# Kernel optimization log

Measured on AMD Instinct MI355X. Metric: run time of the kernel, lower is better.

## Reference

```python
import jax, jax.numpy as jnp
import numpy as np

B, C, IMG, P = 8, 6, 384, 16
DIM, HEADS, DEPTH, MLP, NCLS = 768, 12, 4, 3072, 1000
N = (IMG // P) ** 2            # 576 patches
DH = DIM // HEADS              # 64
PATCH_DIM = C * P * P          # 1536


def setup_inputs() -> dict:
    key = jax.random.key(0)
    ks = jax.random.split(key, 13)
    f = lambda k, shp, s=0.02: jax.random.normal(k, shp, jnp.float32) * s
    return {
        "x": jax.random.normal(ks[0], (B, C, IMG, IMG), jnp.float32),
        "patch_w": f(ks[1], (PATCH_DIM, DIM)),
        "patch_b": f(ks[2], (DIM,)),
        "ln1_g": jnp.ones((DEPTH, DIM), jnp.float32),
        "ln1_b": jnp.zeros((DEPTH, DIM), jnp.float32),
        "w_qkv": f(ks[3], (DEPTH, DIM, 3 * DIM)),
        "bias_att": f(ks[4], (DEPTH, HEADS, N, N), 0.5),
        "w_out": f(ks[5], (DEPTH, DIM, DIM)),
        "ln2_g": jnp.ones((DEPTH, DIM), jnp.float32),
        "ln2_b": jnp.zeros((DEPTH, DIM), jnp.float32),
        "w1": f(ks[6], (DEPTH, DIM, MLP)),
        "b1": f(ks[7], (DEPTH, MLP)),
        "w2": f(ks[8], (DEPTH, MLP, DIM)),
        "b2": f(ks[9], (DEPTH, DIM)),
        "lnh_g": jnp.ones((DIM,), jnp.float32),
        "lnh_b": jnp.zeros((DIM,), jnp.float32),
        "w_head": f(ks[10], (DIM, NCLS)),
        "b_head": f(ks[11], (NCLS,)),
    }


def _ln(x, g, b, eps=1e-5):
    m = x.mean(-1, keepdims=True)
    v = ((x - m) ** 2).mean(-1, keepdims=True)
    return (x - m) * jax.lax.rsqrt(v + eps) * g + b


def _patchify(x, patch_w, patch_b):
    # Rearrange 'b c (h p1) (w p2) -> b (h w) (p1 p2 c)' then Linear(patch_dim, dim)
    b = x.shape[0]
    g = IMG // P
    x = x.reshape(b, C, g, P, g, P).transpose(0, 2, 4, 3, 5, 1).reshape(b, g * g, PATCH_DIM)
    return x @ patch_w + patch_b


def _forward(x, patch_w, patch_b, ln1_g, ln1_b, w_qkv, bias_att, w_out,
             ln2_g, ln2_b, w1, b1, w2, b2, lnh_g, lnh_b, w_head, b_head):
    scale = DH ** -0.5
    tok = _patchify(x, patch_w, patch_b)  # [B, N, DIM]; pos_info='mul_att_normed' -> no pos_embed added

    def block(t, p):
        l1g, l1b, wqkv, bias, wout, l2g, l2b, ww1, bb1, ww2, bb2 = p
        h = _ln(t, l1g, l1b)
        qkv = h @ wqkv                                     # [B, N, 3*DIM]
        q, k, v = jnp.split(qkv, 3, axis=-1)
        rs = lambda a: a.reshape(t.shape[0], N, HEADS, DH).transpose(0, 2, 1, 3)
        q, k, v = rs(q), rs(k), rs(v)                      # [B, H, N, DH]
        dots = jnp.einsum('bhid,bhjd->bhij', q, k) * scale
        # mul_att_normed: softmax(qk) * softmax(bias), renormalized over keys
        attn = jax.nn.softmax(dots, axis=-1) * jax.nn.softmax(bias, axis=-1)[None]
        attn = attn / attn.sum(-1, keepdims=True)
        o = jnp.einsum('bhij,bhjd->bhid', attn, v)
        o = o.transpose(0, 2, 1, 3).reshape(t.shape[0], N, DIM) @ wout
        t = t + o
        h2 = _ln(t, l2g, l2b)
        t = t + (jax.nn.gelu(h2 @ ww1 + bb1, approximate=False) @ ww2 + bb2)
        return t, None

    tok, _ = jax.lax.scan(block, tok,
                          (ln1_g, ln1_b, w_qkv, bias_att, w_out,
                           ln2_g, ln2_b, w1, b1, w2, b2))
    pooled = tok.mean(axis=1)                              # mean-pool tokens
    return _ln(pooled, lnh_g, lnh_b) @ w_head + b_head     # [B, NCLS]


def reference(x, patch_w, patch_b, ln1_g, ln1_b, w_qkv, bias_att, w_out,
              ln2_g, ln2_b, w1, b1, w2, b2, lnh_g, lnh_b, w_head, b_head):
    return _forward(x, patch_w, patch_b, ln1_g, ln1_b, w_qkv, bias_att, w_out,
                    ln2_g, ln2_b, w1, b1, w2, b2, lnh_g, lnh_b, w_head, b_head)
```

## Files before the change

kernel.cpp:

```cpp
#include <hip/hip_runtime.h>
#include <hip/hip_bf16.h>

typedef __attribute__((ext_vector_type(8))) short bf16x8;
typedef __attribute__((ext_vector_type(4))) float f32x4;

#define DEVI __device__ __forceinline__

DEVI unsigned short f2bf_bits(float f) {
    __hip_bfloat16 h = __float2bfloat16(f);
    return *reinterpret_cast<unsigned short*>(&h);
}
DEVI float bfbits2f(unsigned short u) {
    __hip_bfloat16 h = *reinterpret_cast<__hip_bfloat16*>(&u);
    return __bfloat162float(h);
}

DEVI void gload_lds16(const void* g, void* lds) {
    __builtin_amdgcn_global_load_lds(
        (const __attribute__((address_space(1))) unsigned int*)g,
        (__attribute__((address_space(3))) unsigned int*)lds, 16, 0, 0);
}

template <int N> DEVI void wait_vm() {
    if constexpr (N == 0) asm volatile("s_waitcnt vmcnt(0)" ::: "memory");
    else if constexpr (N == 4) asm volatile("s_waitcnt vmcnt(4)" ::: "memory");
    else if constexpr (N == 6) asm volatile("s_waitcnt vmcnt(6)" ::: "memory");
    else if constexpr (N == 12) asm volatile("s_waitcnt vmcnt(12)" ::: "memory");
    __builtin_amdgcn_sched_barrier(0);
}
DEVI void lgkm0() {
    asm volatile("s_waitcnt lgkmcnt(0)" ::: "memory");
    __builtin_amdgcn_sched_barrier(0);
}

DEVI int2 remap2d(int bid, int total, int gx) {
    int q = total >> 3, r = total & 7, x = bid & 7, l = bid >> 3;
    int seq = (x < r ? x * (q + 1) : r * (q + 1) + (x - r) * q) + l;
    int g4 = seq / (4 * gx);
    int rem = seq - g4 * 4 * gx;
    return {g4 * 4 + (rem & 3), rem >> 2};
}
DEVI int2 remap2d_g2(int bid, int total, int gx) {
    int q = total >> 3, r = total & 7, x = bid & 7, l = bid >> 3;
    int seq = (x < r ? x * (q + 1) : r * (q + 1) + (x - r) * q) + l;
    int g2 = seq / (2 * gx);
    int rem = seq - g2 * 2 * gx;
    return {g2 * 2 + (rem & 1), rem >> 1};
}

__global__ __launch_bounds__(256) void patchify_kernel(const float* __restrict__ x,
                                                       unsigned short* __restrict__ patches)
{
    size_t t8 = (size_t)blockIdx.x * 256 + threadIdx.x;
    int jq = (int)(t8 % 48);
    size_t t = t8 / 48;
    int r = (int)(t % 384); t /= 384;
    int c = (int)(t % 6);
    int b = (int)(t / 6);
    int j = jq * 8;
    int gh = r >> 4, p1 = r & 15, gw = j >> 4, p2 = j & 15;
    int prow = b * 576 + gh * 24 + gw;
    int pcol = c * 256 + p1 * 16 + p2;
    const float* src = x + ((((size_t)b * 6 + c) * 384 + r) * 384 + j);
    float4 v0 = ((const float4*)src)[0];
    float4 v1 = ((const float4*)src)[1];
    ushort u[8] = { f2bf_bits(v0.x), f2bf_bits(v0.y), f2bf_bits(v0.z), f2bf_bits(v0.w),
                    f2bf_bits(v1.x), f2bf_bits(v1.y), f2bf_bits(v1.z), f2bf_bits(v1.w) };
    *(int4*)&patches[(size_t)prow * 1536 + pcol] = *(int4*)u;
}

__global__ __launch_bounds__(256) void convT_patch_kernel(const float* __restrict__ W,
                                                          __hip_bfloat16* __restrict__ Wt)
{
    __shared__ float tile[32][33];
    int n0 = blockIdx.x * 32, kp0 = blockIdx.y * 32;
    int tx = threadIdx.x & 31, ty = threadIdx.x >> 5;
#pragma unroll
    for (int i = 0; i < 4; i++) {
        int kp = kp0 + ty + 8 * i;
        int k = (kp & 255) * 6 + (kp >> 8);
        tile[ty + 8 * i][tx] = W[(size_t)k * 768 + n0 + tx];
    }
    __syncthreads();
#pragma unroll
    for (int i = 0; i < 4; i++)
        Wt[(size_t)(n0 + ty + 8 * i) * 1536 + kp0 + tx] = __float2bfloat16(tile[tx][ty + 8 * i]);
}

DEVI void convT4_dispatch(int bt, const float* wqkv, const float* wout,
                          const float* w1, const float* w2,
                          const float* g1, const float* b1ln,
                          const float* g2, const float* b2ln,
                          __hip_bfloat16* dst, float* part, int tid)
{
    const float* W; const float* gv = nullptr; const float* bv = nullptr;
    __hip_bfloat16* Wt; int K, N, lt, nseg = 0;
    if (bt < 1728)      { W = wqkv; K = 768;  N = 2304; lt = bt;        Wt = dst;           gv = g1; bv = b1ln; nseg = 0; }
    else if (bt < 2304) { W = wout; K = 768;  N = 768;  lt = bt - 1728; Wt = dst + 1769472; }
    else if (bt < 4608) { W = w1;   K = 768;  N = 3072; lt = bt - 2304; Wt = dst + 2359296; gv = g2; bv = b2ln; nseg = 2304; }
    else                { W = w2;   K = 3072; N = 768;  lt = bt - 4608; Wt = dst + 4718592; }
    int tn = N >> 5;
    int k0 = (lt / tn) * 32, n0 = (lt % tn) * 32;

    __shared__ float tile[32][33];
    int tx = tid & 31, ty = tid >> 5;
#pragma unroll
    for (int i = 0; i < 4; i++)
        tile[ty + 8 * i][tx] = W[(size_t)(k0 + ty + 8 * i) * N + n0 + tx];
    __syncthreads();
    float gk = gv ? gv[k0 + tx] : 1.0f;
#pragma unroll
    for (int i = 0; i < 4; i++)
        Wt[(size_t)(n0 + ty + 8 * i) * K + k0 + tx] = __float2bfloat16(tile[tx][ty + 8 * i] * gk);
    if (gv && tid < 64) {
        int nn = tid & 31, j = tid >> 5;
        const float* vec = j ? gv : bv;
        float s = 0.f;
#pragma unroll
        for (int kk = 0; kk < 32; kk++) s += vec[k0 + kk] * tile[kk][nn];
        int kt = k0 >> 5;
        part[((size_t)kt * 2 + j) * 5376 + nseg + n0 + nn] = s;
    }
}

__global__ __launch_bounds__(256) void convT4_kernel(const float* __restrict__ wqkv,
                                                     const float* __restrict__ wout,
                                                     const float* __restrict__ w1,
                                                     const float* __restrict__ w2,
                                                     const float* __restrict__ g1,
                                                     const float* __restrict__ b1ln,
                                                     const float* __restrict__ g2,
                                                     const float* __restrict__ b2ln,
                                                     __hip_bfloat16* __restrict__ dst,
                                                     float* __restrict__ part)
{
    convT4_dispatch(blockIdx.x, wqkv, wout, w1, w2, g1, b1ln, g2, b2ln, dst, part, threadIdx.x);
}

__global__ __launch_bounds__(256) void convT4all_kernel(const float* __restrict__ wqkv,
                                                        const float* __restrict__ wout,
                                                        const float* __restrict__ w1,
                                                        const float* __restrict__ w2,
                                                        const float* __restrict__ ln1_g,
                                                        const float* __restrict__ ln1_b,
                                                        const float* __restrict__ ln2_g,
                                                        const float* __restrict__ ln2_b,
                                                        __hip_bfloat16* __restrict__ dst,
                                                        float* __restrict__ part)
{
    int l = blockIdx.x / 6912, bt = blockIdx.x % 6912;
    convT4_dispatch(bt,
                    wqkv + (size_t)l * 768 * 2304, wout + (size_t)l * 768 * 768,
                    w1 + (size_t)l * 768 * 3072, w2 + (size_t)l * 3072 * 768,
                    ln1_g + l * 768, ln1_b + l * 768, ln2_g + l * 768, ln2_b + l * 768,
                    dst + (size_t)l * 7077888, part + (size_t)l * 258048, threadIdx.x);
}

__global__ __launch_bounds__(256) void lnreduce_kernel(const float* __restrict__ part,
                                                       const float* __restrict__ b1,
                                                       float* __restrict__ coef,
                                                       int lbase)
{
    int l = lbase + blockIdx.y;
    const float* p = part + (size_t)blockIdx.y * 258048;
    int n = blockIdx.x * 256 + threadIdx.x;
    float s1 = 0.f, s2 = 0.f;
    for (int kt = 0; kt < 24; kt++) {
        s1 += p[((size_t)kt * 2 + 0) * 5376 + n];
        s2 += p[((size_t)kt * 2 + 1) * 5376 + n];
    }
    float* dst = coef + (size_t)l * 10752;
    if (n < 2304) { dst[n] = s1; dst[2304 + n] = s2; }
    else {
        int n0 = n - 2304;
        dst[4608 + n0] = s1 + b1[(size_t)l * 3072 + n0];
        dst[4608 + 3072 + n0] = s2;
    }
}

__global__ __launch_bounds__(256) void stats_kernel(const __hip_bfloat16* __restrict__ tok,
                                                    float2* __restrict__ stats)
{
    int row = blockIdx.x * 4 + (threadIdx.x >> 6);
    int lane = threadIdx.x & 63;
    const unsigned short* tr = (const unsigned short*)(tok + (size_t)row * 768) + lane * 12;
    float s = 0.f, s2 = 0.f;
#pragma unroll
    for (int i = 0; i < 3; i++) {
        ushort4 u = ((const ushort4*)tr)[i];
        float v0 = bfbits2f(u.x), v1 = bfbits2f(u.y), v2 = bfbits2f(u.z), v3 = bfbits2f(u.w);
        s += v0 + v1 + v2 + v3;
        s2 += v0 * v0 + v1 * v1 + v2 * v2 + v3 * v3;
    }
#pragma unroll
    for (int m = 32; m >= 1; m >>= 1) { s += __shfl_xor(s, m); s2 += __shfl_xor(s2, m); }
    if (lane == 0) {
        float mean = s * (1.0f / 768.0f);
        float var = s2 * (1.0f / 768.0f) - mean * mean;
        stats[row] = make_float2(mean, rsqrtf(var + 1e-5f));
    }
}

__global__ __launch_bounds__(192) void lnf_kernel(const float* __restrict__ x,
                                                  const float* __restrict__ g,
                                                  const float* __restrict__ b,
                                                  float* __restrict__ out)
{
    int row = blockIdx.x, tid = threadIdx.x;
    float4 v4 = *(const float4*)&x[(size_t)row * 768 + tid * 4];
    float v[4] = {v4.x, v4.y, v4.z, v4.w};
    float s = v[0] + v[1] + v[2] + v[3];
    float s2 = v[0] * v[0] + v[1] * v[1] + v[2] * v[2] + v[3] * v[3];
#pragma unroll
    for (int m = 32; m >= 1; m >>= 1) { s += __shfl_xor(s, m); s2 += __shfl_xor(s2, m); }
    __shared__ float red[6];
    int w = tid >> 6;
    if ((tid & 63) == 0) { red[w] = s; red[3 + w] = s2; }
    __syncthreads();
    s = red[0] + red[1] + red[2];
    s2 = red[3] + red[4] + red[5];
    float mean = s * (1.0f / 768.0f);
    float var = s2 * (1.0f / 768.0f) - mean * mean;
    float rstd = rsqrtf(var + 1e-5f);
    float4 g4 = *(const float4*)&g[tid * 4];
    float4 b4 = *(const float4*)&b[tid * 4];
    float o[4] = { (v[0] - mean) * rstd * g4.x + b4.x, (v[1] - mean) * rstd * g4.y + b4.y,
                   (v[2] - mean) * rstd * g4.z + b4.z, (v[3] - mean) * rstd * g4.w + b4.w };
    *(float4*)&out[(size_t)row * 768 + tid * 4] = make_float4(o[0], o[1], o[2], o[3]);
}

template <bool GELU>
__global__ __launch_bounds__(512, 2) void gemm_8ph_kernel(
    const __hip_bfloat16* __restrict__ A,
    const __hip_bfloat16* __restrict__ Bt,
    const float2* __restrict__ stats,
    const float* __restrict__ c1v,
    const float* __restrict__ c2v,
    __hip_bfloat16* __restrict__ Cb,
    int M, int N, int K, int gx)
{
    __shared__ __align__(16) __hip_bfloat16 AsF[32768];
    __shared__ __align__(16) __hip_bfloat16 BsF[32768];
    const int tid = threadIdx.x;
    const int wid = tid >> 6, lane = tid & 63;
    const int g = lane >> 4, l16 = lane & 15;
    const int wmh = wid >> 2, wnn = wid & 3;

    int2 bc = remap2d_g2(blockIdx.x, gridDim.x, gx);
    const int bm = bc.x * 256, bn = bc.y * 256;

    const int srow = tid >> 2;
    size_t aS[2], bS[2];
#pragma unroll
    for (int i = 0; i < 2; i++) {
        int row = i * 128 + srow;
        int lc = (tid & 3) ^ ((row >> 1) & 3);
        aS[i] = (size_t)(bm + row) * K + lc * 8;
        bS[i] = (size_t)(bn + row) * K + lc * 8;
    }
    auto stageA = [&](int buf, int kh, int tq) {
        const __hip_bfloat16* ap = A + (size_t)tq * 64 + kh * 32;
        __hip_bfloat16* dst = AsF + (buf * 2 + kh) * 8192;
        gload_lds16(ap + aS[0], dst + tid * 8);
        gload_lds16(ap + aS[1], dst + 4096 + tid * 8);
    };
    auto stageB = [&](int buf, int kh, int tq) {
        const __hip_bfloat16* bp = Bt + (size_t)tq * 64 + kh * 32;
        __hip_bfloat16* dst = BsF + (buf * 2 + kh) * 8192;
        gload_lds16(bp + bS[0], dst + tid * 8);
        gload_lds16(bp + bS[1], dst + 4096 + tid * 8);
    };

    const int csw = (l16 >> 1) & 3;
    const int rdo = (g ^ csw) << 3;
    const int aBase = (wmh * 128 + l16) * 32 + rdo;
    const int bBase = (wnn * 64 + l16) * 32 + rdo;

    f32x4 acc[8][4] = {};
    const int nt = K >> 6;

    stageA(0, 0, 0); stageB(0, 0, 0); stageA(0, 1, 0); stageB(0, 1, 0);
    stageA(1, 0, 1); stageB(1, 0, 1);
    wait_vm<4>();
    __builtin_amdgcn_s_barrier();
    __builtin_amdgcn_sched_barrier(0);

    bf16x8 af[8], bf2[2];
    for (int t = 0; t < nt; t++) {
        const int b = t & 1;
        const int k0 = (b * 2 + 0) * 8192, k1 = (b * 2 + 1) * 8192;

#pragma unroll
        for (int mi = 0; mi < 8; mi++) af[mi] = *(const bf16x8*)&AsF[k0 + aBase + mi * 512];
        bf2[0] = *(const bf16x8*)&BsF[k0 + bBase + 0 * 512];
        bf2[1] = *(const bf16x8*)&BsF[k0 + bBase + 1 * 512];
        if (t + 1 < nt) stageA(b ^ 1, 1, t + 1);
        __builtin_amdgcn_s_barrier(); lgkm0();
        __builtin_amdgcn_s_setprio(1);
#pragma unroll
        for (int mi = 0; mi < 8; mi++) {
            acc[mi][0] = __builtin_amdgcn_mfma_f32_16x16x32_bf16(af[mi], bf2[0], acc[mi][0], 0, 0, 0);
            acc[mi][1] = __builtin_amdgcn_mfma_f32_16x16x32_bf16(af[mi], bf2[1], acc[mi][1], 0, 0, 0);
        }
        __builtin_amdgcn_s_setprio(0);
        __builtin_amdgcn_s_barrier();

        bf2[0] = *(const bf16x8*)&BsF[k0 + bBase + 2 * 512];
        bf2[1] = *(const bf16x8*)&BsF[k0 + bBase + 3 * 512];
        if (t + 1 < nt) stageB(b ^ 1, 1, t + 1);
        __builtin_amdgcn_s_barrier(); lgkm0();
        __builtin_amdgcn_s_setprio(1);
#pragma unroll
        for (int mi = 0; mi < 8; mi++) {
            acc[mi][2] = __builtin_amdgcn_mfma_f32_16x16x32_bf16(af[mi], bf2[0], acc[mi][2], 0, 0, 0);
            acc[mi][3] = __builtin_amdgcn_mfma_f32_16x16x32_bf16(af[mi], bf2[1], acc[mi][3], 0, 0, 0);
        }
        __builtin_amdgcn_s_setprio(0);
        __builtin_amdgcn_s_barrier();

#pragma unroll
        for (int mi = 0; mi < 8; mi++) af[mi] = *(const bf16x8*)&AsF[k1 + aBase + mi * 512];
        bf2[0] = *(const bf16x8*)&BsF[k1 + bBase + 0 * 512];
        bf2[1] = *(const bf16x8*)&BsF[k1 + bBase + 1 * 512];
        if (t + 2 < nt) stageA(b, 0, t + 2);
        __builtin_amdgcn_s_barrier(); lgkm0();
        __builtin_amdgcn_s_setprio(1);
#pragma unroll
        for (int mi = 0; mi < 8; mi++) {
            acc[mi][0] = __builtin_amdgcn_mfma_f32_16x16x32_bf16(af[mi], bf2[0], acc[mi][0], 0, 0, 0);
            acc[mi][1] = __builtin_amdgcn_mfma_f32_16x16x32_bf16(af[mi], bf2[1], acc[mi][1], 0, 0, 0);
        }
        __builtin_amdgcn_s_setprio(0);
        __builtin_amdgcn_s_barrier();

        bf2[0] = *(const bf16x8*)&BsF[k1 + bBase + 2 * 512];
        bf2[1] = *(const bf16x8*)&BsF[k1 + bBase + 3 * 512];
        if (t + 2 < nt) stageB(b, 0, t + 2);
        __builtin_amdgcn_s_barrier(); lgkm0();
        __builtin_amdgcn_s_setprio(1);
#pragma unroll
        for (int mi = 0; mi < 8; mi++) {
            acc[mi][2] = __builtin_amdgcn_mfma_f32_16x16x32_bf16(af[mi], bf2[0], acc[mi][2], 0, 0, 0);
            acc[mi][3] = __builtin_amdgcn_mfma_f32_16x16x32_bf16(af[mi], bf2[1], acc[mi][3], 0, 0, 0);
        }
        __builtin_amdgcn_s_setprio(0);
        if (t + 2 < nt) wait_vm<4>();
        else            wait_vm<0>();
        __builtin_amdgcn_s_barrier();
        __builtin_amdgcn_sched_barrier(0);
    }

    __hip_bfloat16* scr = AsF + wid * (16 * 72);
#pragma unroll
    for (int mi = 0; mi < 8; mi++) {
        float2 st[4];
#pragma unroll
        for (int r = 0; r < 4; r++)
            st[r] = stats[bm + wmh * 128 + mi * 16 + 4 * g + r];
#pragma unroll
        for (int ni = 0; ni < 4; ni++) {
            int gcol = bn + wnn * 64 + ni * 16 + l16;
            float c1 = c1v[gcol], c2 = c2v[gcol];
#pragma unroll
            for (int r = 0; r < 4; r++) {
                float v = st[r].y * (acc[mi][ni][r] - st[r].x * c2) + c1;
                if (GELU) v = 0.5f * v * (1.0f + erff(v * 0.70710678118654752f));
                scr[(4 * g + r) * 72 + ni * 16 + l16] = __float2bfloat16(v);
            }
        }
        lgkm0();
#pragma unroll
        for (int q2 = 0; q2 < 2; q2++) {
            int idx = q2 * 64 + lane;
            int row16 = idx >> 3, ch = idx & 7;
            bf16x8 vv = *(const bf16x8*)&scr[row16 * 72 + ch * 8];
            int grow = bm + wmh * 128 + mi * 16 + row16;
            *(int4*)&Cb[(size_t)grow * N + bn + wnn * 64 + ch * 8] = *(int4*)&vv;
        }
        lgkm0();
    }
}

template <bool BIAS, bool RESID, bool GELU>
__global__ __launch_bounds__(256, 2) void gemm_bt_kernel(
    const __hip_bfloat16* __restrict__ A,
    const __hip_bfloat16* __restrict__ Bt,
    const float* __restrict__ bias,
    const __hip_bfloat16* __restrict__ resid,
    __hip_bfloat16* __restrict__ Cb,
    int M, int N, int K, int gx)
{
    constexpr int BM = 64;
    __shared__ __align__(16) __hip_bfloat16 As[3][BM * 64];
    __shared__ __align__(16) __hip_bfloat16 Bs[3][128 * 64];
    const int tid = threadIdx.x;
    const int wid = tid >> 6, lane = tid & 63;
    const int g = lane >> 4, l16 = lane & 15;
    const int wm = (wid >> 1) * 32, wn = (wid & 1) * 64;

    int2 bc = remap2d(blockIdx.x, gridDim.x, gx);
    const int bm = bc.x * BM, bn = bc.y * 128;

    const int sr32 = tid >> 3, ci = tid & 7;
    const int cg = ci ^ (sr32 & 7);
    const int sdst = tid * 8;
    size_t aOff[2], bOff[4];
#pragma unroll
    for (int i = 0; i < 2; i++) aOff[i] = (size_t)(bm + i * 32 + sr32) * K + cg * 8;
#pragma unroll
    for (int i = 0; i < 4; i++) bOff[i] = (size_t)(bn + i * 32 + sr32) * K + cg * 8;

    auto stage = [&](__hip_bfloat16* asb, __hip_bfloat16* bsb, int tq) {
        const __hip_bfloat16* ap = A + tq * 64;
        const __hip_bfloat16* bp = Bt + tq * 64;
#pragma unroll
        for (int i = 0; i < 2; i++) gload_lds16(ap + aOff[i], asb + i * 2048 + sdst);
#pragma unroll
        for (int i = 0; i < 4; i++) gload_lds16(bp + bOff[i], bsb + i * 2048 + sdst);
    };

    f32x4 acc[2][4] = {};
    const int nt = K >> 6;

    stage(As[0], Bs[0], 0);
    stage(As[1], Bs[1], 1);
    stage(As[2], Bs[2], 2);
    wait_vm<12>();
    __builtin_amdgcn_s_barrier();
    __builtin_amdgcn_sched_barrier(0);

    for (int t = 0; t < nt; t += 3) {
#pragma unroll
        for (int u = 0; u < 3; u++) {
            const int tc = t + u;
            bf16x8 af[2][2], bfr[2][4];
#pragma unroll
            for (int s = 0; s < 2; s++) {
                const int cp = ((s * 4 + g) ^ (l16 & 7)) << 3;
#pragma unroll
                for (int mi = 0; mi < 2; mi++)
                    af[s][mi] = *(const bf16x8*)&As[u][(wm + mi * 16 + l16) * 64 + cp];
#pragma unroll
                for (int ni = 0; ni < 4; ni++)
                    bfr[s][ni] = *(const bf16x8*)&Bs[u][(wn + ni * 16 + l16) * 64 + cp];
            }
#pragma unroll
            for (int s = 0; s < 2; s++)
#pragma unroll
                for (int mi = 0; mi < 2; mi++)
#pragma unroll
                    for (int ni = 0; ni < 4; ni++)
                        acc[mi][ni] = __builtin_amdgcn_mfma_f32_16x16x32_bf16(af[s][mi], bfr[s][ni], acc[mi][ni], 0, 0, 0);

            lgkm0();
            __builtin_amdgcn_s_barrier();
            __builtin_amdgcn_sched_barrier(0);

            if (tc + 3 < nt) stage(As[u], Bs[u], tc + 3);
            if (tc + 1 < nt) {
                if (tc + 4 <= nt)      wait_vm<12>();
                else if (tc + 3 == nt) wait_vm<6>();
                else                   wait_vm<0>();
                __builtin_amdgcn_s_barrier();
                __builtin_amdgcn_sched_barrier(0);
            }
        }
    }

    __hip_bfloat16* scr = &As[0][0] + wid * (16 * 72);
#pragma unroll
    for (int mi = 0; mi < 2; mi++) {
#pragma unroll
        for (int ni = 0; ni < 4; ni++) {
            float bval = 0.0f;
            if (BIAS) bval = bias[bn + wn + ni * 16 + l16];
#pragma unroll
            for (int r = 0; r < 4; r++) {
                float v = acc[mi][ni][r] + bval;
                if (GELU) v = 0.5f * v * (1.0f + erff(v * 0.70710678118654752f));
                scr[(4 * g + r) * 72 + ni * 16 + l16] = __float2bfloat16(v);
            }
        }
        lgkm0();
#pragma unroll
        for (int q2 = 0; q2 < 2; q2++) {
            int row16 = q2 * 8 + (lane >> 3), ch = lane & 7;
            bf16x8 vv = *(const bf16x8*)&scr[row16 * 72 + ch * 8];
            int grow = bm + wm + mi * 16 + row16;
            size_t off = (size_t)grow * N + bn + wn + ch * 8;
            if (RESID) {
                bf16x8 rv = *(const bf16x8*)&resid[off];
#pragma unroll
                for (int e = 0; e < 8; e++)
                    vv[e] = (short)f2bf_bits(bfbits2f((unsigned short)vv[e]) + bfbits2f((unsigned short)rv[e]));
            }
            *(int4*)&Cb[off] = *(int4*)&vv;
        }
        lgkm0();
    }
}

__global__ __launch_bounds__(256) void attn_kernel(const __hip_bfloat16* __restrict__ qkvb,
                                                   const float* __restrict__ bias,
                                                   unsigned short* __restrict__ o)
{
    const int seq = (blockIdx.x & 7) * 108 + (blockIdx.x >> 3);
    const int bb = seq & 7, qt = (seq >> 3) % 9, h = seq / 72;
    const int q0 = qt * 64;
    const int tid = threadIdx.x;
    const int wq = tid >> 6, lane = tid & 63, g = lane >> 4, l16 = lane & 15;

    __shared__ __align__(16) unsigned short Qs[64 * 72];
    __shared__ __align__(16) unsigned short Ks[64 * 72];
    __shared__ __align__(16) unsigned short Vt[64 * 72];
    __shared__ __align__(16) unsigned short Ps[4][16 * 72];

    {
        int r = tid >> 2, cb = (tid & 3) * 16;
        const int4* s4 = (const int4*)&qkvb[(size_t)(bb * 576 + q0 + r) * 2304 + h * 64 + cb];
        int4* d4 = (int4*)&Qs[r * 72 + cb];
        d4[0] = s4[0]; d4[1] = s4[1];
    }
    __syncthreads();
    bf16x8 qf0 = *(const bf16x8*)&Qs[(wq * 16 + l16) * 72 + g * 8];
    bf16x8 qf1 = *(const bf16x8*)&Qs[(wq * 16 + l16) * 72 + 32 + g * 8];

    float m_r[4] = {-1e30f, -1e30f, -1e30f, -1e30f};
    float l_r[4] = {0.f, 0.f, 0.f, 0.f};
    f32x4 oa[4] = {};
    const float* bias_h = bias + (size_t)h * 576 * 576;
    const float scale = 0.125f;

    for (int kt = 0; kt < 576; kt += 64) {
        {
            int r = tid >> 2, cb = (tid & 3) * 16;
            const int4* s4 = (const int4*)&qkvb[(size_t)(bb * 576 + kt + r) * 2304 + 768 + h * 64 + cb];
            int4* d4 = (int4*)&Ks[r * 72 + cb];
            d4[0] = s4[0]; d4[1] = s4[1];
            int key = tid & 63, d0 = (tid >> 6) * 16;
            const unsigned short* vs = (const unsigned short*)&qkvb[(size_t)(bb * 576 + kt + key) * 2304 + 1536 + h * 64 + d0];
            bf16x8 v0 = *(const bf16x8*)vs;
            bf16x8 v1 = *(const bf16x8*)(vs + 8);
#pragma unroll
            for (int e = 0; e < 8; e++) {
                Vt[(d0 + e) * 72 + key] = (unsigned short)v0[e];
                Vt[(d0 + 8 + e) * 72 + key] = (unsigned short)v1[e];
            }
        }
        __syncthreads();

        float bl[4][4];
#pragma unroll
        for (int kc = 0; kc < 4; kc++)
#pragma unroll
            for (int r = 0; r < 4; r++) {
                int q = q0 + wq * 16 + 4 * g + r;
                bl[kc][r] = bias_h[(size_t)q * 576 + kt + kc * 16 + l16];
            }

        f32x4 sc[4] = {};
        __builtin_amdgcn_s_setprio(1);
#pragma unroll
        for (int kc = 0; kc < 4; kc++) {
            bf16x8 kf0 = *(const bf16x8*)&Ks[(kc * 16 + l16) * 72 + g * 8];
            bf16x8 kf1 = *(const bf16x8*)&Ks[(kc * 16 + l16) * 72 + 32 + g * 8];
            sc[kc] = __builtin_amdgcn_mfma_f32_16x16x32_bf16(qf0, kf0, sc[kc], 0, 0, 0);
            sc[kc] = __builtin_amdgcn_mfma_f32_16x16x32_bf16(qf1, kf1, sc[kc], 0, 0, 0);
        }
        __builtin_amdgcn_s_setprio(0);

        float sv[4][4], mt[4] = {-1e30f, -1e30f, -1e30f, -1e30f};
#pragma unroll
        for (int kc = 0; kc < 4; kc++)
#pragma unroll
            for (int r = 0; r < 4; r++) {
                float s = sc[kc][r] * scale + bl[kc][r];
                sv[kc][r] = s;
                mt[r] = fmaxf(mt[r], s);
            }
#pragma unroll
        for (int r = 0; r < 4; r++)
#pragma unroll
            for (int m = 1; m < 16; m <<= 1) mt[r] = fmaxf(mt[r], __shfl_xor(mt[r], m));

        float sf[4];
#pragma unroll
        for (int r = 0; r < 4; r++) {
            float mn = fmaxf(m_r[r], mt[r]);
            sf[r] = __expf(m_r[r] - mn);
            m_r[r] = mn;
        }
        float rs[4] = {0.f, 0.f, 0.f, 0.f};
#pragma unroll
        for (int kc = 0; kc < 4; kc++)
#pragma unroll
            for (int r = 0; r < 4; r++) {
                float p = __expf(sv[kc][r] - m_r[r]);
                rs[r] += p;
                Ps[wq][(4 * g + r) * 72 + kc * 16 + l16] = f2bf_bits(p);
            }
#pragma unroll
        for (int r = 0; r < 4; r++) {
#pragma unroll
            for (int m = 1; m < 16; m <<= 1) rs[r] += __shfl_xor(rs[r], m);
            l_r[r] = l_r[r] * sf[r] + rs[r];
        }
#pragma unroll
        for (int dt = 0; dt < 4; dt++)
#pragma unroll
            for (int r = 0; r < 4; r++) oa[dt][r] *= sf[r];

        asm volatile("s_waitcnt lgkmcnt(0)" ::: "memory");

        __builtin_amdgcn_s_setprio(1);
#pragma unroll
        for (int s = 0; s < 2; s++) {
            bf16x8 pf = *(const bf16x8*)&Ps[wq][l16 * 72 + s * 32 + g * 8];
#pragma unroll
            for (int dt = 0; dt < 4; dt++) {
                bf16x8 vf = *(const bf16x8*)&Vt[(dt * 16 + l16) * 72 + s * 32 + g * 8];
                oa[dt] = __builtin_amdgcn_mfma_f32_16x16x32_bf16(pf, vf, oa[dt], 0, 0, 0);
            }
        }
        __builtin_amdgcn_s_setprio(0);
        __syncthreads();
    }

#pragma unroll
    for (int dt = 0; dt < 4; dt++)
#pragma unroll
        for (int r = 0; r < 4; r++) {
            int q = q0 + wq * 16 + 4 * g + r;
            float v = oa[dt][r] / l_r[r];
            o[(size_t)(bb * 576 + q) * 768 + h * 64 + dt * 16 + l16] = f2bf_bits(v);
        }
}

__global__ __launch_bounds__(256) void pool_kernel(const __hip_bfloat16* __restrict__ tok,
                                                   float* __restrict__ pooled)
{
    int d = blockIdx.x * 256 + threadIdx.x;
    int b = blockIdx.y;
    float s = 0.0f;
    for (int n = 0; n < 576; n++) s += __bfloat162float(tok[(size_t)(b * 576 + n) * 768 + d]);
    pooled[b * 768 + d] = s * (1.0f / 576.0f);
}

__global__ __launch_bounds__(256) void head_kernel(const float* __restrict__ lnp,
                                                   const float* __restrict__ w,
                                                   const float* __restrict__ bh,
                                                   float* __restrict__ out)
{
    int c = blockIdx.x * 256 + threadIdx.x;
    int b = blockIdx.y;
    if (c >= 1000) return;
    float s = bh[c];
    for (int d = 0; d < 768; d++) s += lnp[b * 768 + d] * w[(size_t)d * 1000 + c];
    out[b * 1000 + c] = s;
}

extern "C" void kernel_launch(void* const* d_in, const int* in_sizes, int n_in,
                              void* d_out, int out_size, void* d_ws, size_t ws_size,
                              hipStream_t stream)
{
    const float* x = (const float*)d_in[0];
    const float* patch_w = (const float*)d_in[1];
    const float* patch_b = (const float*)d_in[2];
    const float* ln1_g = (const float*)d_in[3];
    const float* ln1_b = (const float*)d_in[4];
    const float* w_qkv = (const float*)d_in[5];
    const float* bias_att = (const float*)d_in[6];
    const float* w_out = (const float*)d_in[7];
    const float* ln2_g = (const float*)d_in[8];
    const float* ln2_b = (const float*)d_in[9];
    const float* w1 = (const float*)d_in[10];
    const float* b1 = (const float*)d_in[11];
    const float* w2 = (const float*)d_in[12];
    const float* b2 = (const float*)d_in[13];
    const float* lnh_g = (const float*)d_in[14];
    const float* lnh_b = (const float*)d_in[15];
    const float* w_head = (const float*)d_in[16];
    const float* b_head = (const float*)d_in[17];
    float* out = (float*)d_out;

    char* ws = (char*)d_ws;
    __hip_bfloat16* tok = (__hip_bfloat16*)(ws + 0);
    __hip_bfloat16* qkv_bf = (__hip_bfloat16*)(ws + 14155776);
    float* coef = (float*)(ws + 35389440);
    float2* stats = (float2*)(ws + 35561856);
    float* part = (float*)(ws + 35717120);
    float* pooled = (float*)(ws + 56623104);
    float* pooledln = (float*)(ws + 56647680);
    __hip_bfloat16* patches = (__hip_bfloat16*)(ws + 56672256);
    __hip_bfloat16* lw = patches;
    __hip_bfloat16* o_bf = (__hip_bfloat16*)(ws + 77905920);
    __hip_bfloat16* hid_bf = (__hip_bfloat16*)(ws + 84983808);
    __hip_bfloat16* wbuf = (__hip_bfloat16*)(ws + 113295360);
    __hip_bfloat16* lwAll = (__hip_bfloat16*)(ws + 118013952);
    const bool useAll = ws_size >= (size_t)118013952 + 56623104;

    patchify_kernel<<<3456, 256, 0, stream>>>(x, (unsigned short*)patches);
    convT_patch_kernel<<<dim3(24, 48), 256, 0, stream>>>(patch_w, wbuf);
    gemm_bt_kernel<true, false, false><<<432, 256, 0, stream>>>(
        patches, wbuf, patch_b, nullptr, tok, 4608, 768, 1536, 6);

    if (useAll) {
        convT4all_kernel<<<27648, 256, 0, stream>>>(
            w_qkv, w_out, w1, w2, ln1_g, ln1_b, ln2_g, ln2_b, lwAll, part);
        lnreduce_kernel<<<dim3(21, 4), 256, 0, stream>>>(part, b1, coef, 0);
    }

    for (int l = 0; l < 4; l++) {
        __hip_bfloat16* lwl = useAll ? lwAll + (size_t)l * 7077888 : lw;
        const float* cf = coef + (size_t)l * 10752;
        if (!useAll) {
            convT4_kernel<<<6912, 256, 0, stream>>>(
                w_qkv + (size_t)l * 768 * 2304, w_out + (size_t)l * 768 * 768,
                w1 + (size_t)l * 768 * 3072, w2 + (size_t)l * 3072 * 768,
                ln1_g + l * 768, ln1_b + l * 768, ln2_g + l * 768, ln2_b + l * 768, lw, part);
            lnreduce_kernel<<<dim3(21, 1), 256, 0, stream>>>(part, b1, coef, l);
        }
        stats_kernel<<<1152, 256, 0, stream>>>(tok, stats);
        gemm_8ph_kernel<false><<<162, 512, 0, stream>>>(
            tok, lwl, stats, cf, cf + 2304, qkv_bf, 4608, 2304, 768, 9);
        attn_kernel<<<864, 256, 0, stream>>>(
            qkv_bf, bias_att + (size_t)l * 12 * 576 * 576, (unsigned short*)o_bf);
        gemm_bt_kernel<false, true, false><<<432, 256, 0, stream>>>(
            o_bf, lwl + 1769472, nullptr, tok, tok, 4608, 768, 768, 6);
        stats_kernel<<<1152, 256, 0, stream>>>(tok, stats);
        gemm_8ph_kernel<true><<<216, 512, 0, stream>>>(
            tok, lwl + 2359296, stats, cf + 4608, cf + 4608 + 3072, hid_bf, 4608, 3072, 768, 12);
        gemm_bt_kernel<true, true, false><<<432, 256, 0, stream>>>(
            hid_bf, lwl + 4718592, b2 + l * 768, tok, tok, 4608, 768, 3072, 6);
    }

    pool_kernel<<<dim3(3, 8), 256, 0, stream>>>(tok, pooled);
    lnf_kernel<<<8, 192, 0, stream>>>(pooled, lnh_g, lnh_b, pooledln);
    head_kernel<<<dim3(4, 8), 256, 0, stream>>>(pooledln, w_head, b_head, out);
}
```

Before: 840.8 us.

## Fuse LayerNorm row statistics into GEMM A-fragment loop, drop stats kernel

Removes the standalone stats_kernel launches before the QKV and MLP-up GEMMs. Wave column 0 of each workgroup accumulates row sum and sum-of-squares from the A fragments it already loads, reduces them across lane groups, and stores per-row mean/rstd in LDS for the epilogue. This saves two launches and one read of the token tensor per layer. In exchange it adds VALU work on one wave per phase, which can stall the other waves at the barriers, plus an extra syncthreads before the epilogue.

```diff
diff --git a/kernel.cpp b/kernel.cpp
--- a/kernel.cpp
+++ b/kernel.cpp
@@ -178,29 +178,6 @@
     }
 }
 
-__global__ __launch_bounds__(256) void stats_kernel(const __hip_bfloat16* __restrict__ tok,
-                                                    float2* __restrict__ stats)
-{
-    int row = blockIdx.x * 4 + (threadIdx.x >> 6);
-    int lane = threadIdx.x & 63;
-    const unsigned short* tr = (const unsigned short*)(tok + (size_t)row * 768) + lane * 12;
-    float s = 0.f, s2 = 0.f;
-#pragma unroll
-    for (int i = 0; i < 3; i++) {
-        ushort4 u = ((const ushort4*)tr)[i];
-        float v0 = bfbits2f(u.x), v1 = bfbits2f(u.y), v2 = bfbits2f(u.z), v3 = bfbits2f(u.w);
-        s += v0 + v1 + v2 + v3;
-        s2 += v0 * v0 + v1 * v1 + v2 * v2 + v3 * v3;
-    }
-#pragma unroll
-    for (int m = 32; m >= 1; m >>= 1) { s += __shfl_xor(s, m); s2 += __shfl_xor(s2, m); }
-    if (lane == 0) {
-        float mean = s * (1.0f / 768.0f);
-        float var = s2 * (1.0f / 768.0f) - mean * mean;
-        stats[row] = make_float2(mean, rsqrtf(var + 1e-5f));
-    }
-}
-
 __global__ __launch_bounds__(192) void lnf_kernel(const float* __restrict__ x,
                                                   const float* __restrict__ g,
                                                   const float* __restrict__ b,
@@ -233,7 +210,6 @@
 __global__ __launch_bounds__(512, 2) void gemm_8ph_kernel(
     const __hip_bfloat16* __restrict__ A,
     const __hip_bfloat16* __restrict__ Bt,
-    const float2* __restrict__ stats,
     const float* __restrict__ c1v,
     const float* __restrict__ c2v,
     __hip_bfloat16* __restrict__ Cb,
@@ -277,6 +253,7 @@
     const int bBase = (wnn * 64 + l16) * 32 + rdo;
 
     f32x4 acc[8][4] = {};
+    float s1a[8] = {}, s2a[8] = {};
     const int nt = K >> 6;
 
     stageA(0, 0, 0); stageB(0, 0, 0); stageA(0, 1, 0); stageB(0, 1, 0);
@@ -303,6 +280,18 @@
             acc[mi][1] = __builtin_amdgcn_mfma_f32_16x16x32_bf16(af[mi], bf2[1], acc[mi][1], 0, 0, 0);
         }
         __builtin_amdgcn_s_setprio(0);
+        if (wnn == 0) {
+#pragma unroll
+            for (int mi = 0; mi < 8; mi++) {
+                float a = 0.f, bb2 = 0.f;
+#pragma unroll
+                for (int e = 0; e < 8; e++) {
+                    float v = bfbits2f((unsigned short)af[mi][e]);
+                    a += v; bb2 += v * v;
+                }
+                s1a[mi] += a; s2a[mi] += bb2;
+            }
+        }
         __builtin_amdgcn_s_barrier();
 
         bf2[0] = *(const bf16x8*)&BsF[k0 + bBase + 2 * 512];
@@ -331,6 +320,18 @@
             acc[mi][1] = __builtin_amdgcn_mfma_f32_16x16x32_bf16(af[mi], bf2[1], acc[mi][1], 0, 0, 0);
         }
         __builtin_amdgcn_s_setprio(0);
+        if (wnn == 0) {
+#pragma unroll
+            for (int mi = 0; mi < 8; mi++) {
+                float a = 0.f, bb2 = 0.f;
+#pragma unroll
+                for (int e = 0; e < 8; e++) {
+                    float v = bfbits2f((unsigned short)af[mi][e]);
+                    a += v; bb2 += v * v;
+                }
+                s1a[mi] += a; s2a[mi] += bb2;
+            }
+        }
         __builtin_amdgcn_s_barrier();
 
         bf2[0] = *(const bf16x8*)&BsF[k1 + bBase + 2 * 512];
@@ -350,13 +351,29 @@
         __builtin_amdgcn_sched_barrier(0);
     }
 
+    float2* sRow = (float2*)BsF;
+    if (wnn == 0) {
+#pragma unroll
+        for (int mi = 0; mi < 8; mi++) {
+            float a = s1a[mi], b2 = s2a[mi];
+            a += __shfl_xor(a, 16); a += __shfl_xor(a, 32);
+            b2 += __shfl_xor(b2, 16); b2 += __shfl_xor(b2, 32);
+            if (g == 0) {
+                float mean = a * (1.0f / 768.0f);
+                float var = b2 * (1.0f / 768.0f) - mean * mean;
+                sRow[wmh * 128 + mi * 16 + l16] = make_float2(mean, rsqrtf(var + 1e-5f));
+            }
+        }
+    }
+    __syncthreads();
+
     __hip_bfloat16* scr = AsF + wid * (16 * 72);
 #pragma unroll
     for (int mi = 0; mi < 8; mi++) {
         float2 st[4];
 #pragma unroll
         for (int r = 0; r < 4; r++)
-            st[r] = stats[bm + wmh * 128 + mi * 16 + 4 * g + r];
+            st[r] = sRow[wmh * 128 + mi * 16 + 4 * g + r];
 #pragma unroll
         for (int ni = 0; ni < 4; ni++) {
             int gcol = bn + wnn * 64 + ni * 16 + l16;
@@ -687,7 +704,6 @@
     __hip_bfloat16* tok = (__hip_bfloat16*)(ws + 0);
     __hip_bfloat16* qkv_bf = (__hip_bfloat16*)(ws + 14155776);
     float* coef = (float*)(ws + 35389440);
-    float2* stats = (float2*)(ws + 35561856);
     float* part = (float*)(ws + 35717120);
     float* pooled = (float*)(ws + 56623104);
     float* pooledln = (float*)(ws + 56647680);
@@ -720,16 +736,14 @@
                 ln1_g + l * 768, ln1_b + l * 768, ln2_g + l * 768, ln2_b + l * 768, lw, part);
             lnreduce_kernel<<<dim3(21, 1), 256, 0, stream>>>(part, b1, coef, l);
         }
-        stats_kernel<<<1152, 256, 0, stream>>>(tok, stats);
         gemm_8ph_kernel<false><<<162, 512, 0, stream>>>(
-            tok, lwl, stats, cf, cf + 2304, qkv_bf, 4608, 2304, 768, 9);
+            tok, lwl, cf, cf + 2304, qkv_bf, 4608, 2304, 768, 9);
         attn_kernel<<<864, 256, 0, stream>>>(
             qkv_bf, bias_att + (size_t)l * 12 * 576 * 576, (unsigned short*)o_bf);
         gemm_bt_kernel<false, true, false><<<432, 256, 0, stream>>>(
             o_bf, lwl + 1769472, nullptr, tok, tok, 4608, 768, 768, 6);
-        stats_kernel<<<1152, 256, 0, stream>>>(tok, stats);
         gemm_8ph_kernel<true><<<216, 512, 0, stream>>>(
-            tok, lwl + 2359296, stats, cf + 4608, cf + 4608 + 3072, hid_bf, 4608, 3072, 768, 12);
+            tok, lwl + 2359296, cf + 4608, cf + 4608 + 3072, hid_bf, 4608, 3072, 768, 12);
         gemm_bt_kernel<true, true, false><<<432, 256, 0, stream>>>(
             hid_bf, lwl + 4718592, b2 + l * 768, tok, tok, 4608, 768, 3072, 6);
     }
```

New measurement: 961.3 us. +14.3%, slower.
